# Optimization experiments

Hardware: AMD Instinct MI355X
Metric: run time of the kernel (lower is better)

## Reference

```python
import jax, jax.numpy as jnp
import numpy as np

B, N, C, H, NC = 8, 4096, 512, 256, 1000
GRID = 64  # N = GRID*GRID unique positions
LN_EPS = 1e-5


def setup_inputs() -> dict:
    key = jax.random.key(0)
    ks = jax.random.split(key, 10)
    # unique integer grid positions, same for every batch element (original order)
    i = jnp.arange(N)
    base = jnp.stack([i % GRID, i // GRID], axis=-1).astype(jnp.float32)  # [N,2]
    pos_org = jnp.broadcast_to(base, (B, N, 2))
    # per-batch random permutation -> shuffled positions (as the backbone would emit)
    perm = jax.vmap(lambda k: jax.random.permutation(k, N))(jax.random.split(ks[0], B))  # [B,N]
    pos_shuffled = jnp.take_along_axis(pos_org, perm[..., None], axis=1)
    s = 0.02
    return {
        "feat": jax.random.normal(ks[1], (B, N, C), jnp.float32),
        "prev_out": jax.random.normal(ks[2], (B, N, C), jnp.float32),
        "pos_org": pos_org,
        "pos_shuffled": pos_shuffled,
        "proj_W": jax.random.normal(ks[3], (C, C), jnp.float32) * s,
        "proj_b": jnp.zeros((C,), jnp.float32),
        "ln_g": jnp.ones((C,), jnp.float32),
        "ln_b": jnp.zeros((C,), jnp.float32),
        "W1": jax.random.normal(ks[4], (H, C), jnp.float32) * s,
        "b1": jnp.zeros((H,), jnp.float32),
        "W2": jax.random.normal(ks[5], (H, H), jnp.float32) * s,
        "b2": jnp.zeros((H,), jnp.float32),
        "W3": jax.random.normal(ks[6], (NC, H), jnp.float32) * s,
        "b3": jnp.zeros((NC,), jnp.float32),
    }


def _layernorm(x, g, b):
    x32 = x.astype(jnp.float32)
    mu = x32.mean(-1, keepdims=True)
    var = ((x32 - mu) ** 2).mean(-1, keepdims=True)
    return (x32 - mu) * jax.lax.rsqrt(var + LN_EPS) * g + b


def reference(feat, prev_out, pos_org, pos_shuffled, proj_W, proj_b,
              ln_g, ln_b, W1, b1, W2, b2, W3, b3):
    # find_pos_org_order: L1 cdist [B,N,N] + argmin over shuffled axis
    dists = jnp.abs(pos_org[:, :, None, :] - pos_shuffled[:, None, :, :]).sum(-1)
    pos_indices = jnp.argmin(dists, axis=2)  # [B,N]
    # batched gather: feat[b_, pos_indices]
    g = jnp.take_along_axis(feat, pos_indices[..., None], axis=1)  # [B,N,C]
    # fused proj -> layernorm (in fp32) -> cast back -> residual add
    proj = jnp.einsum('bnc,dc->bnd', g, proj_W) + proj_b
    out_feat = prev_out + _layernorm(proj, ln_g, ln_b).astype(feat.dtype)
    # mean-pool over tokens, 3-layer MLP head with relu on first two layers
    pooled = out_feat.mean(1)  # [B,C]
    h = jax.nn.relu(pooled @ W1.T + b1)
    h = jax.nn.relu(h @ W2.T + b2)
    return h @ W3.T + b3  # [B, num_classes]
```

## Files before the change

### kernel.cpp

```cpp
#include <hip/hip_runtime.h>
#include <stdint.h>

#define B_ 8
#define N_ 4096
#define C_ 512
#define H_ 256
#define NC_ 1000

typedef float v4f __attribute__((ext_vector_type(4)));
typedef short v8s __attribute__((ext_vector_type(8)));
typedef unsigned short ushort_t;

__device__ __forceinline__ uint32_t f2bf1(float f) {
    uint32_t u = __float_as_uint(f);
    return (u + 0x7FFFu + ((u >> 16) & 1u)) >> 16;
}
__device__ __forceinline__ uint32_t pk2(float lo, float hi) {
#if __has_builtin(__builtin_amdgcn_cvt_pk_bf16_f32)
    auto r = __builtin_amdgcn_cvt_pk_bf16_f32(lo, hi);
    return __builtin_bit_cast(uint32_t, r);
#else
    return f2bf1(lo) | (f2bf1(hi) << 16);
#endif
}

__global__ void prep_kernel(const float* __restrict__ ps, const float* __restrict__ W,
                            int* __restrict__ inv, ushort_t* __restrict__ Wfrag,
                            float* __restrict__ pooled) {
    int blk = blockIdx.x, t = threadIdx.x;
    if (blk == 0) {
        float4 z = {0.f, 0.f, 0.f, 0.f};
#pragma unroll
        for (int i = 0; i < 4; i++) ((float4*)pooled)[t * 4 + i] = z;
    }
    if (blk < 128) {
        int gid = blk * 256 + t;
        float2 p = ((const float2*)ps)[gid];
        int key = (int)(p.x + 0.5f) + 64 * (int)(p.y + 0.5f);
        int b = gid >> 12;
        inv[(b << 12) + key] = gid & 4095;
    } else {
        int i = (blk - 128) * 256 + t;
        int d = i >> 6, kb = (i >> 2) & 15, q = i & 3;
        const float4* src = (const float4*)(W + d * C_ + kb * 32 + q * 8);
        float4 v0 = src[0], v1 = src[1];
        uint4 pk;
        pk.x = pk2(v0.x, v0.y); pk.y = pk2(v0.z, v0.w);
        pk.z = pk2(v1.x, v1.y); pk.w = pk2(v1.z, v1.w);
        ((uint4*)Wfrag)[((d >> 4) * 16 + kb) * 64 + q * 16 + (d & 15)] = pk;
    }
}

__global__ __launch_bounds__(512, 4)
void gemm_ln_pool(const float* __restrict__ feat, const float* __restrict__ prev,
                  const int* __restrict__ inv, const ushort_t* __restrict__ Wfrag,
                  const float* __restrict__ pb, const float* __restrict__ lg,
                  const float* __restrict__ lb, float* __restrict__ pooled) {
    __shared__ v8s Abuf[4096];
    __shared__ float RowS[64], RowQ[64], ColS[512];

    const int bid = blockIdx.x;
    const int t = threadIdx.x;

    if (bid % 3 == 2) {
        const int p = bid / 3;
        const int b = p >> 5;
        const int r0 = (p & 31) << 7;
        const float* psrc = prev + ((size_t)(b * N_ + r0) * C_) + t;
        float s0 = 0.f, s1 = 0.f, s2 = 0.f, s3 = 0.f;
#pragma unroll 4
        for (int r = 0; r < 128; r += 4) {
            s0 += __builtin_nontemporal_load(&psrc[(r + 0) * C_]);
            s1 += __builtin_nontemporal_load(&psrc[(r + 1) * C_]);
            s2 += __builtin_nontemporal_load(&psrc[(r + 2) * C_]);
            s3 += __builtin_nontemporal_load(&psrc[(r + 3) * C_]);
        }
        atomicAdd(&pooled[b * C_ + t], (s0 + s1) + (s2 + s3));
        return;
    }

    const int gix = (bid / 3) * 2 + (bid % 3);
    const int b = gix >> 6;
    const int row0 = (gix & 63) << 6;
    const int wv = t >> 6, lane = t & 63, c = lane & 15, q = lane >> 4;

    if (t < 64) { RowS[t] = 0.f; RowQ[t] = 0.f; }

    const int arow = t >> 3;
    const int acol8 = t & 7;
    const int grow = inv[(b << 12) + row0 + arow];
    const v4f* asrc = (const v4f*)(feat + ((size_t)(b * N_ + grow) * C_));
#pragma unroll 4
    for (int s = 0; s < 8; s++) {
        const int chunk = s * 8 + acol8;
        v4f f0 = __builtin_nontemporal_load(asrc + chunk * 2);
        v4f f1 = __builtin_nontemporal_load(asrc + chunk * 2 + 1);
        uint4 pk;
        pk.x = pk2(f0.x, f0.y); pk.y = pk2(f0.z, f0.w);
        pk.z = pk2(f1.x, f1.y); pk.w = pk2(f1.z, f1.w);
        ((uint4*)Abuf)[arow * 64 + (chunk ^ (arow & 7))] = pk;
    }

    const ushort_t* fb[4];
#pragma unroll
    for (int nt = 0; nt < 4; nt++)
        fb[nt] = Wfrag + (wv * 4 + nt) * 8192 + lane * 8;

    v4f acc[4][4];
    const v4f vzero = {0.f, 0.f, 0.f, 0.f};
#pragma unroll
    for (int mt = 0; mt < 4; mt++)
#pragma unroll
        for (int nt = 0; nt < 4; nt++) acc[mt][nt] = vzero;

    __syncthreads();

#pragma unroll 2
    for (int kb = 0; kb < 16; kb++) {
        v8s af[4], bf[4];
#pragma unroll
        for (int nt = 0; nt < 4; nt++)
            bf[nt] = *((const v8s*)(fb[nt] + kb * 512));
#pragma unroll
        for (int mt = 0; mt < 4; mt++)
            af[mt] = Abuf[(mt * 16 + c) * 64 + ((kb * 4 + q) ^ (c & 7))];
#pragma unroll
        for (int mt = 0; mt < 4; mt++)
#pragma unroll
            for (int nt = 0; nt < 4; nt++)
                acc[mt][nt] = __builtin_amdgcn_mfma_f32_16x16x32_bf16(
                    af[mt], bf[nt], acc[mt][nt], 0, 0, 0);
    }

    float pb4[4], lg4[4], lb4[4];
#pragma unroll
    for (int nt = 0; nt < 4; nt++) {
        int n = wv * 64 + nt * 16 + c;
        pb4[nt] = pb[n]; lg4[nt] = lg[n]; lb4[nt] = lb[n];
    }
#pragma unroll
    for (int mt = 0; mt < 4; mt++) {
#pragma unroll
        for (int reg = 0; reg < 4; reg++) {
            float s1 = 0.f, s2 = 0.f;
#pragma unroll
            for (int nt = 0; nt < 4; nt++) {
                float v = acc[mt][nt][reg] + pb4[nt];
                acc[mt][nt][reg] = v;
                s1 += v; s2 += v * v;
            }
#pragma unroll
            for (int d = 1; d < 16; d <<= 1) {
                s1 += __shfl_xor(s1, d);
                s2 += __shfl_xor(s2, d);
            }
            if (c == 0) {
                int r = mt * 16 + q * 4 + reg;
                atomicAdd(&RowS[r], s1);
                atomicAdd(&RowQ[r], s2);
            }
        }
    }
    __syncthreads();
    if (t < 64) {
        float mu = RowS[t] * (1.f / C_);
        float var = RowQ[t] * (1.f / C_) - mu * mu;
        RowS[t] = mu;
        RowQ[t] = rsqrtf(var + 1e-5f);
    }
    __syncthreads();
    float col[4] = {0.f, 0.f, 0.f, 0.f};
#pragma unroll
    for (int mt = 0; mt < 4; mt++) {
#pragma unroll
        for (int reg = 0; reg < 4; reg++) {
            int r = mt * 16 + q * 4 + reg;
            float mu = RowS[r], rs = RowQ[r];
#pragma unroll
            for (int nt = 0; nt < 4; nt++)
                col[nt] += (acc[mt][nt][reg] - mu) * rs * lg4[nt] + lb4[nt];
        }
    }
#pragma unroll
    for (int nt = 0; nt < 4; nt++) {
        col[nt] += __shfl_xor(col[nt], 16);
        col[nt] += __shfl_xor(col[nt], 32);
    }
    if (lane < 16) {
#pragma unroll
        for (int nt = 0; nt < 4; nt++) ColS[wv * 64 + nt * 16 + c] = col[nt];
    }
    __syncthreads();
    atomicAdd(&pooled[b * C_ + t], ColS[t]);
}

__global__ __launch_bounds__(256)
void head_kernel(const float* __restrict__ pooled,
                 const float* __restrict__ W1, const float* __restrict__ b1,
                 const float* __restrict__ W2, const float* __restrict__ b2,
                 const float* __restrict__ W3, const float* __restrict__ b3,
                 float* __restrict__ out) {
    __shared__ __align__(16) float P[512];
    __shared__ __align__(16) float H1[256];
    __shared__ __align__(16) float H2[256];
    const int t = threadIdx.x, wv = t >> 6, lane = t & 63;
    const int b = blockIdx.x / 25;
    const int slice = blockIdx.x % 25;

    P[t] = pooled[b * C_ + t] * (1.f / 4096.f);
    P[t + 256] = pooled[b * C_ + t + 256] * (1.f / 4096.f);
    __syncthreads();

    {
        const float4* wr = (const float4*)(W1 + t * C_);
        float s = 0.f;
#pragma unroll 8
        for (int k = 0; k < 128; k++) {
            float4 w = wr[k];
            float4 p = ((const float4*)P)[k];
            s += w.x * p.x + w.y * p.y + w.z * p.z + w.w * p.w;
        }
        H1[t] = fmaxf(s + b1[t], 0.f);
    }
    __syncthreads();

    {
        const float4* wr = (const float4*)(W2 + t * H_);
        float s = 0.f;
#pragma unroll 8
        for (int k = 0; k < 64; k++) {
            float4 w = wr[k];
            float4 p = ((const float4*)H1)[k];
            s += w.x * p.x + w.y * p.y + w.z * p.z + w.w * p.w;
        }
        H2[t] = fmaxf(s + b2[t], 0.f);
    }
    __syncthreads();

#pragma unroll
    for (int jj = 0; jj < 10; jj++) {
        const int o = slice * 40 + jj * 4 + wv;
        float4 w = ((const float4*)(W3 + o * H_))[lane];
        float4 p = ((const float4*)H2)[lane];
        float s = w.x * p.x + w.y * p.y + w.z * p.z + w.w * p.w;
#pragma unroll
        for (int d = 1; d < 64; d <<= 1) s += __shfl_xor(s, d);
        if (lane == 0) out[b * NC_ + o] = s + b3[o];
    }
}

extern "C" void kernel_launch(void* const* d_in, const int* in_sizes, int n_in,
                              void* d_out, int out_size, void* d_ws, size_t ws_size,
                              hipStream_t stream) {
    const float* feat  = (const float*)d_in[0];
    const float* prev  = (const float*)d_in[1];
    const float* ps    = (const float*)d_in[3];
    const float* projW = (const float*)d_in[4];
    const float* pb    = (const float*)d_in[5];
    const float* lg    = (const float*)d_in[6];
    const float* lb    = (const float*)d_in[7];
    const float* W1    = (const float*)d_in[8];
    const float* b1    = (const float*)d_in[9];
    const float* W2    = (const float*)d_in[10];
    const float* b2    = (const float*)d_in[11];
    const float* W3    = (const float*)d_in[12];
    const float* b3    = (const float*)d_in[13];
    float* out = (float*)d_out;

    char* ws = (char*)d_ws;
    ushort_t* Wfrag = (ushort_t*)ws;
    int* inv        = (int*)(ws + 524288);
    float* pooled   = (float*)(ws + 655360);

    prep_kernel<<<256, 256, 0, stream>>>(ps, projW, inv, Wfrag, pooled);
    gemm_ln_pool<<<768, 512, 0, stream>>>(feat, prev, inv, Wfrag,
                                          pb, lg, lb, pooled);
    head_kernel<<<200, 256, 0, stream>>>(pooled, W1, b1, W2, b2, W3, b3, out);
}
```

Baseline: 217.7 us.

## Split prev_out pooling into separate vectorized kernel after GEMM

Moves the prev_out column-sum out of the fused GEMM/LN kernel, where it ran in interleaved blocks, into its own kernel launched after the GEMM. The new kernel uses 16-byte vector loads with 16 loads in flight per thread and 32-row chunks, so each pass makes fuller use of memory bandwidth. The GEMM grid shrinks to 512 blocks that all do matmul work. The cost is an extra launch, the loss of overlap between pooling and GEMM, and four times as many atomics per column.

```diff
diff --git a/kernel.cpp b/kernel.cpp
--- a/kernel.cpp
+++ b/kernel.cpp
@@ -51,8 +51,34 @@
     }
 }
 
+__global__ __launch_bounds__(256)
+void prev_pool(const float* __restrict__ prev, float* __restrict__ pooled) {
+    const int t = threadIdx.x;
+    const int blk = blockIdx.x;
+    const int b = blk >> 7;
+    const int r0 = (blk & 127) << 5;
+    const int col4 = t & 127, rg = t >> 7;
+    const v4f* psrc =
+        (const v4f*)(prev + (size_t)(b * N_ + r0 + rg * 16) * C_) + col4;
+    v4f v[16];
+#pragma unroll
+    for (int r = 0; r < 16; r++)
+        v[r] = __builtin_nontemporal_load(psrc + (size_t)r * 128);
+    v4f s0 = v[0], s1 = v[1], s2 = v[2], s3 = v[3];
+#pragma unroll
+    for (int r = 4; r < 16; r += 4) {
+        s0 += v[r]; s1 += v[r + 1]; s2 += v[r + 2]; s3 += v[r + 3];
+    }
+    v4f s = (s0 + s1) + (s2 + s3);
+    float* dst = pooled + b * C_ + col4 * 4;
+    atomicAdd(dst + 0, s.x);
+    atomicAdd(dst + 1, s.y);
+    atomicAdd(dst + 2, s.z);
+    atomicAdd(dst + 3, s.w);
+}
+
 __global__ __launch_bounds__(512, 4)
-void gemm_ln_pool(const float* __restrict__ feat, const float* __restrict__ prev,
+void gemm_ln_pool(const float* __restrict__ feat,
                   const int* __restrict__ inv, const ushort_t* __restrict__ Wfrag,
                   const float* __restrict__ pb, const float* __restrict__ lg,
                   const float* __restrict__ lb, float* __restrict__ pooled) {
@@ -61,27 +87,8 @@
 
     const int bid = blockIdx.x;
     const int t = threadIdx.x;
-
-    if (bid % 3 == 2) {
-        const int p = bid / 3;
-        const int b = p >> 5;
-        const int r0 = (p & 31) << 7;
-        const float* psrc = prev + ((size_t)(b * N_ + r0) * C_) + t;
-        float s0 = 0.f, s1 = 0.f, s2 = 0.f, s3 = 0.f;
-#pragma unroll 4
-        for (int r = 0; r < 128; r += 4) {
-            s0 += __builtin_nontemporal_load(&psrc[(r + 0) * C_]);
-            s1 += __builtin_nontemporal_load(&psrc[(r + 1) * C_]);
-            s2 += __builtin_nontemporal_load(&psrc[(r + 2) * C_]);
-            s3 += __builtin_nontemporal_load(&psrc[(r + 3) * C_]);
-        }
-        atomicAdd(&pooled[b * C_ + t], (s0 + s1) + (s2 + s3));
-        return;
-    }
-
-    const int gix = (bid / 3) * 2 + (bid % 3);
-    const int b = gix >> 6;
-    const int row0 = (gix & 63) << 6;
+    const int b = bid >> 6;
+    const int row0 = (bid & 63) << 6;
     const int wv = t >> 6, lane = t & 63, c = lane & 15, q = lane >> 4;
 
     if (t < 64) { RowS[t] = 0.f; RowQ[t] = 0.f; }
@@ -273,7 +280,7 @@
     float* pooled   = (float*)(ws + 655360);
 
     prep_kernel<<<256, 256, 0, stream>>>(ps, projW, inv, Wfrag, pooled);
-    gemm_ln_pool<<<768, 512, 0, stream>>>(feat, prev, inv, Wfrag,
-                                          pb, lg, lb, pooled);
+    gemm_ln_pool<<<512, 512, 0, stream>>>(feat, inv, Wfrag, pb, lg, lb, pooled);
+    prev_pool<<<1024, 256, 0, stream>>>(prev, pooled);
     head_kernel<<<200, 256, 0, stream>>>(pooled, W1, b1, W2, b2, W3, b3, out);
 }
```

After: 260.3 us. 1.2x slower.

## Replace atomic pooling with per-block partials and a deterministic reduce kernel

Applied to the files above, without the earlier changes.

GEMM blocks and prev-sum blocks no longer atomically add into the pooled buffer. Each now writes per-block partial column sums to workspace, and a new small reduce kernel sums them per batch, so pooled no longer needs zeroing in prep. The prev-sum blocks also switch to float4 loads with 4 row groups combined through shared memory, which gives more loads in flight per thread. The cost is an extra kernel launch and a serial reduction over 96 partial rows per batch.

```diff
diff --git a/kernel.cpp b/kernel.cpp
--- a/kernel.cpp
+++ b/kernel.cpp
@@ -25,14 +25,8 @@
 }
 
 __global__ void prep_kernel(const float* __restrict__ ps, const float* __restrict__ W,
-                            int* __restrict__ inv, ushort_t* __restrict__ Wfrag,
-                            float* __restrict__ pooled) {
+                            int* __restrict__ inv, ushort_t* __restrict__ Wfrag) {
     int blk = blockIdx.x, t = threadIdx.x;
-    if (blk == 0) {
-        float4 z = {0.f, 0.f, 0.f, 0.f};
-#pragma unroll
-        for (int i = 0; i < 4; i++) ((float4*)pooled)[t * 4 + i] = z;
-    }
     if (blk < 128) {
         int gid = blk * 256 + t;
         float2 p = ((const float2*)ps)[gid];
@@ -55,9 +49,11 @@
 void gemm_ln_pool(const float* __restrict__ feat, const float* __restrict__ prev,
                   const int* __restrict__ inv, const ushort_t* __restrict__ Wfrag,
                   const float* __restrict__ pb, const float* __restrict__ lg,
-                  const float* __restrict__ lb, float* __restrict__ pooled) {
+                  const float* __restrict__ lb,
+                  float* __restrict__ partialG,
+                  float* __restrict__ partialP) {
     __shared__ v8s Abuf[4096];
-    __shared__ float RowS[64], RowQ[64], ColS[512];
+    __shared__ float RowS[64], RowQ[64];
 
     const int bid = blockIdx.x;
     const int t = threadIdx.x;
@@ -66,16 +62,25 @@
         const int p = bid / 3;
         const int b = p >> 5;
         const int r0 = (p & 31) << 7;
-        const float* psrc = prev + ((size_t)(b * N_ + r0) * C_) + t;
-        float s0 = 0.f, s1 = 0.f, s2 = 0.f, s3 = 0.f;
-#pragma unroll 4
-        for (int r = 0; r < 128; r += 4) {
-            s0 += __builtin_nontemporal_load(&psrc[(r + 0) * C_]);
-            s1 += __builtin_nontemporal_load(&psrc[(r + 1) * C_]);
-            s2 += __builtin_nontemporal_load(&psrc[(r + 2) * C_]);
-            s3 += __builtin_nontemporal_load(&psrc[(r + 3) * C_]);
-        }
-        atomicAdd(&pooled[b * C_ + t], (s0 + s1) + (s2 + s3));
+        const int col4 = t & 127, rg = t >> 7;
+        const v4f* psrc =
+            (const v4f*)(prev + (size_t)(b * N_ + r0 + rg * 32) * C_) + col4;
+        v4f a0 = {0.f, 0.f, 0.f, 0.f}, a1 = a0, a2 = a0, a3 = a0;
+#pragma unroll
+        for (int batch = 0; batch < 4; batch++) {
+            v4f v[8];
+#pragma unroll
+            for (int j = 0; j < 8; j++)
+                v[j] = __builtin_nontemporal_load(psrc + (batch * 8 + j) * 128);
+            a0 += v[0]; a1 += v[1]; a2 += v[2]; a3 += v[3];
+            a0 += v[4]; a1 += v[5]; a2 += v[6]; a3 += v[7];
+        }
+        v4f s = (a0 + a1) + (a2 + a3);
+        float* AbufF = (float*)Abuf;
+        ((v4f*)AbufF)[rg * 128 + col4] = s;
+        __syncthreads();
+        partialP[(size_t)p * 512 + t] =
+            (AbufF[t] + AbufF[512 + t]) + (AbufF[1024 + t] + AbufF[1536 + t]);
         return;
     }
 
@@ -188,10 +193,34 @@
     }
     if (lane < 16) {
 #pragma unroll
-        for (int nt = 0; nt < 4; nt++) ColS[wv * 64 + nt * 16 + c] = col[nt];
-    }
-    __syncthreads();
-    atomicAdd(&pooled[b * C_ + t], ColS[t]);
+        for (int nt = 0; nt < 4; nt++)
+            partialG[(size_t)gix * 512 + wv * 64 + nt * 16 + c] = col[nt];
+    }
+}
+
+__global__ __launch_bounds__(512)
+void reduce_pool(const float* __restrict__ partialG,
+                 const float* __restrict__ partialP,
+                 float* __restrict__ pooled) {
+    const int b = blockIdx.x, t = threadIdx.x;
+    const float* pg = partialG + (size_t)b * 64 * 512 + t;
+    const float* pp = partialP + (size_t)b * 32 * 512 + t;
+    float s0 = 0.f, s1 = 0.f, s2 = 0.f, s3 = 0.f;
+#pragma unroll 4
+    for (int i = 0; i < 64; i += 4) {
+        s0 += pg[(i + 0) * 512];
+        s1 += pg[(i + 1) * 512];
+        s2 += pg[(i + 2) * 512];
+        s3 += pg[(i + 3) * 512];
+    }
+#pragma unroll 4
+    for (int i = 0; i < 32; i += 4) {
+        s0 += pp[(i + 0) * 512];
+        s1 += pp[(i + 1) * 512];
+        s2 += pp[(i + 2) * 512];
+        s3 += pp[(i + 3) * 512];
+    }
+    pooled[b * C_ + t] = (s0 + s1) + (s2 + s3);
 }
 
 __global__ __launch_bounds__(256)
@@ -268,12 +297,15 @@
     float* out = (float*)d_out;
 
     char* ws = (char*)d_ws;
-    ushort_t* Wfrag = (ushort_t*)ws;
-    int* inv        = (int*)(ws + 524288);
-    float* pooled   = (float*)(ws + 655360);
-
-    prep_kernel<<<256, 256, 0, stream>>>(ps, projW, inv, Wfrag, pooled);
+    ushort_t* Wfrag  = (ushort_t*)ws;
+    int* inv         = (int*)(ws + 524288);
+    float* partialG  = (float*)(ws + 655360);
+    float* partialP  = (float*)(ws + 1703936);
+    float* pooled    = (float*)(ws + 2228224);
+
+    prep_kernel<<<256, 256, 0, stream>>>(ps, projW, inv, Wfrag);
     gemm_ln_pool<<<768, 512, 0, stream>>>(feat, prev, inv, Wfrag,
-                                          pb, lg, lb, pooled);
+                                          pb, lg, lb, partialG, partialP);
+    reduce_pool<<<8, 512, 0, stream>>>(partialG, partialP, pooled);
     head_kernel<<<200, 256, 0, stream>>>(pooled, W1, b1, W2, b2, W3, b3, out);
 }
```

Result: no change. 221.0 us (+1.5%).
